# Optimization experiments

Hardware: AMD Instinct MI355X
Metric: run time of the kernel (lower is better)

## Reference

```python
import jax, jax.numpy as jnp
import numpy as np

B, N, K, C_IN, OC = 16, 4096, 16, 64, 64
OC2 = OC // 2
LEAK = 0.2
EPS = 1e-12  # guards sqrt grad when a neighbor equals the center point


def _cbn(x, w, s, b):
    # 1x1 conv (channel-last) + folded eval-mode BatchNorm: (x @ w.T) * s + b
    return jnp.einsum('...i,oi->...o', x, w) * s + b


def _lrelu(x):
    return jax.nn.leaky_relu(x, LEAK)


def _gather(feat, idx):
    # feat [B,N,C], idx [B,N,k] -> [B,N,k,C]  (index_points)
    return jax.vmap(lambda f, i: f[i])(feat, idx)


def _attentive_pool(x_info, feat, idx, wq, sq, bq, wk, sk, bk, wv, sv, bv, w2, s2, b2):
    q = jax.nn.relu(_cbn(feat, wq, sq, bq))   # [B,N,C]
    kf = jax.nn.relu(_cbn(feat, wk, sk, bk))
    vf = jax.nn.relu(_cbn(feat, wv, sv, bv))
    Kn = _gather(kf, idx)                     # [B,N,k,C]
    W = x_info * (Kn - q[:, :, None, :])      # [B,N,k,C]
    Vn = _gather(vf, idx)
    a = jax.nn.softmax(W, axis=2)             # softmax over k neighbors
    out = jnp.sum(a * Vn, axis=2)             # [B,N,C]
    return _lrelu(_cbn(out, w2, s2, b2))


def _forward(x, feature, neighbor_index,
             mlp1_w, mlp1_s, mlp1_b, lse1_w, lse1_s, lse1_b,
             p1_wq, p1_sq, p1_bq, p1_wk, p1_sk, p1_bk, p1_wv, p1_sv, p1_bv, p1_w2, p1_s2, p1_b2,
             lse2_w, lse2_s, lse2_b,
             p2_wq, p2_sq, p2_bq, p2_wk, p2_sk, p2_bk, p2_wv, p2_sv, p2_bv, p2_w2, p2_s2, p2_b2,
             mlp2_w, mlp2_s, mlp2_b, res_w, res_s, res_b):
    idx = neighbor_index
    xt = jnp.transpose(x, (0, 2, 1))          # [B,N,3]
    ft = jnp.transpose(feature, (0, 2, 1))    # [B,N,C_IN]
    identity = ft
    f1 = _lrelu(_cbn(ft, mlp1_w, mlp1_s, mlp1_b))        # [B,N,OC2]
    knn_x = _gather(xt, idx)                             # [B,N,k,3]
    center = jnp.broadcast_to(xt[:, :, None, :], knn_x.shape)
    diff = knn_x - center
    dist = jnp.sqrt(jnp.sum(diff * diff, axis=-1, keepdims=True) + EPS)  # [B,N,k,1]
    x_info = jnp.concatenate([center, knn_x, diff, dist], axis=-1)       # [B,N,k,10]
    x_info = _lrelu(_cbn(x_info, lse1_w, lse1_s, lse1_b))                # [B,N,k,OC2]
    feat2 = _attentive_pool(x_info, f1, idx,
                            p1_wq, p1_sq, p1_bq, p1_wk, p1_sk, p1_bk,
                            p1_wv, p1_sv, p1_bv, p1_w2, p1_s2, p1_b2)    # [B,N,OC2]
    x_info2 = _lrelu(_cbn(x_info, lse2_w, lse2_s, lse2_b))               # [B,N,k,OC2]
    feat3 = _attentive_pool(x_info2, feat2, idx,
                            p2_wq, p2_sq, p2_bq, p2_wk, p2_sk, p2_bk,
                            p2_wv, p2_sv, p2_bv, p2_w2, p2_s2, p2_b2)    # [B,N,OC]
    out = _cbn(feat3, mlp2_w, mlp2_s, mlp2_b)            # [B,N,2*OC]
    res = _cbn(identity, res_w, res_s, res_b)            # [B,N,2*OC]
    out = _lrelu(out + res)
    return jnp.transpose(out, (0, 2, 1))                 # [B,2*OC,N]


def setup_inputs() -> dict:
    key = jax.random.key(0)
    it = iter(jax.random.split(key, 80))
    nxt = lambda: next(it)

    def w(*shape):
        return jax.random.normal(nxt(), shape, jnp.float32) * 0.1

    def bn(c):
        s = jax.random.uniform(nxt(), (c,), jnp.float32, 0.5, 1.5)
        b = jax.random.normal(nxt(), (c,), jnp.float32) * 0.1
        return s, b

    inp = {
        'x': jax.random.normal(nxt(), (B, 3, N), jnp.float32),
        'feature': jax.random.normal(nxt(), (B, C_IN, N), jnp.float32),
        'neighbor_index': jax.random.randint(nxt(), (B, N, K), 0, N, jnp.int32),
    }
    inp['mlp1_w'] = w(OC2, C_IN); inp['mlp1_s'], inp['mlp1_b'] = bn(OC2)
    inp['lse1_w'] = w(OC2, 10); inp['lse1_s'], inp['lse1_b'] = bn(OC2)
    for p, co in (('p1', OC2), ('p2', OC)):
        inp[p + '_wq'] = w(OC2, OC2); inp[p + '_sq'], inp[p + '_bq'] = bn(OC2)
        inp[p + '_wk'] = w(OC2, OC2); inp[p + '_sk'], inp[p + '_bk'] = bn(OC2)
        inp[p + '_wv'] = w(OC2, OC2); inp[p + '_sv'], inp[p + '_bv'] = bn(OC2)
        inp[p + '_w2'] = w(co, OC2); inp[p + '_s2'], inp[p + '_b2'] = bn(co)
    inp['lse2_w'] = w(OC2, OC2); inp['lse2_s'], inp['lse2_b'] = bn(OC2)
    inp['mlp2_w'] = w(2 * OC, OC); inp['mlp2_s'], inp['mlp2_b'] = bn(2 * OC)
    inp['res_w'] = w(2 * OC, C_IN); inp['res_s'], inp['res_b'] = bn(2 * OC)
    return inp


def reference(x, feature, neighbor_index,
              mlp1_w, mlp1_s, mlp1_b, lse1_w, lse1_s, lse1_b,
              p1_wq, p1_sq, p1_bq, p1_wk, p1_sk, p1_bk, p1_wv, p1_sv, p1_bv, p1_w2, p1_s2, p1_b2,
              lse2_w, lse2_s, lse2_b,
              p2_wq, p2_sq, p2_bq, p2_wk, p2_sk, p2_bk, p2_wv, p2_sv, p2_bv, p2_w2, p2_s2, p2_b2,
              mlp2_w, mlp2_s, mlp2_b, res_w, res_s, res_b):
    return _forward(x, feature, neighbor_index,
                    mlp1_w, mlp1_s, mlp1_b, lse1_w, lse1_s, lse1_b,
                    p1_wq, p1_sq, p1_bq, p1_wk, p1_sk, p1_bk, p1_wv, p1_sv, p1_bv, p1_w2, p1_s2, p1_b2,
                    lse2_w, lse2_s, lse2_b,
                    p2_wq, p2_sq, p2_bq, p2_wk, p2_sk, p2_bk, p2_wv, p2_sv, p2_bv, p2_w2, p2_s2, p2_b2,
                    mlp2_w, mlp2_s, mlp2_b, res_w, res_s, res_b)
```

## Files before the change

### kernel.cpp

```cpp
#include <hip/hip_runtime.h>
#include <cstdint>
#include <cstddef>

#define NB 16
#define NP 4096
#define KNN 16
#define CIN 64
#define H 32
#define OCC 64
#define PN ((size_t)NB*NP)

__device__ __forceinline__ float lrelu(float v){ return v > 0.f ? v : 0.2f*v; }
__device__ __forceinline__ float reluf(float v){ return v > 0.f ? v : 0.f; }

typedef __attribute__((ext_vector_type(8)))  short bf16x8s;
typedef __attribute__((ext_vector_type(4)))  float f32x4;
typedef __attribute__((ext_vector_type(16))) float f32x16;

__device__ __forceinline__ short f2bf(float f){
    union { float f; unsigned u; } v; v.f = f;
    unsigned r = v.u + 0x7fffu + ((v.u >> 16) & 1u);
    return (short)(r >> 16);
}

__global__ __launch_bounds__(256) void k_pointwise(
    const float* __restrict__ feat, const float* __restrict__ xpos,
    const float* __restrict__ w1, const float* __restrict__ s1, const float* __restrict__ b1,
    const float* __restrict__ wq, const float* __restrict__ sq, const float* __restrict__ bq,
    const float* __restrict__ wk, const float* __restrict__ sk, const float* __restrict__ bk,
    const float* __restrict__ wv, const float* __restrict__ sv, const float* __restrict__ bv,
    float* __restrict__ q1, float* __restrict__ kv1,
    float* __restrict__ xp, short* __restrict__ ftp,
    const float* __restrict__ m2w, const float* __restrict__ m2s, const float* __restrict__ m2b,
    const float* __restrict__ rw, const float* __restrict__ rs, const float* __restrict__ rb,
    const float* __restrict__ p2w2,
    short* __restrict__ wbigW, short* __restrict__ w2bW, float* __restrict__ bbW)
{
    __shared__ unsigned short ftb[64*72];
    __shared__ unsigned short f1b[64*40];
    int t = threadIdx.x;
    int l = t & 63;
    int g = t >> 6;
    int bid = blockIdx.x;
    int b  = bid >> 6;
    int n0 = (bid & 63) * 64;
    int n  = n0 + l;
    size_t p = (size_t)b*NP + n;

    {
        const float* fb = feat + ((size_t)b*CIN)*NP + n;
        float fv[16];
        #pragma unroll
        for (int k=0;k<16;k++) fv[k] = fb[(size_t)(g*16+k)*NP];
        bf16x8s h0, h1;
        #pragma unroll
        for (int i=0;i<8;i++){ h0[i] = f2bf(fv[i]); h1[i] = f2bf(fv[8+i]); }
        *(bf16x8s*)(ftp + p*64 + g*16)     = h0;
        *(bf16x8s*)(ftp + p*64 + g*16 + 8) = h1;
        *(bf16x8s*)&ftb[l*72 + g*16]       = h0;
        *(bf16x8s*)&ftb[l*72 + g*16 + 8]   = h1;
    }
    if (g == 0){
        const float* xb = xpos + (size_t)b*3*NP;
        *(float4*)(xp + 4*p) = make_float4(xb[n], xb[NP+n], xb[2*NP+n], 0.f);
    }
    if (bid == 0){
        int o = t >> 1, half = t & 1;
        const float* srcp = half ? (rw + (size_t)o*64) : (m2w + (size_t)o*64);
        float sc = half ? rs[o] : m2s[o];
        short* dst = wbigW + (size_t)o*128 + half*64;
        #pragma unroll
        for (int j=0;j<64;j+=8){
            bf16x8s v8;
            #pragma unroll
            for (int i=0;i<8;i++) v8[i] = f2bf(srcp[j+i]*sc);
            *(bf16x8s*)(dst + j) = v8;
        }
        if (!half) bbW[o] = m2b[o] + rb[o];
        {
            int i0 = t*8;
            bf16x8s w8;
            #pragma unroll
            for (int i=0;i<8;i++) w8[i] = f2bf(p2w2[i0+i]);
            *(bf16x8s*)(w2bW + i0) = w8;
        }
    }
    __syncthreads();

    int lr = t & 15;
    int kg = (t >> 4) & 3;
    int prow = g*16 + lr;
    size_t pg = (size_t)b*NP + n0 + prow;

    f32x4 Df0 = {0.f,0.f,0.f,0.f}, Df1 = {0.f,0.f,0.f,0.f};
    #pragma unroll
    for (int kk=0; kk<2; kk++){
        bf16x8s Bf = *(const bf16x8s*)&ftb[prow*72 + kk*32 + kg*8];
        {
            int h = lr;
            float sc = s1[h];
            const float* wr = w1 + h*64 + kk*32 + kg*8;
            bf16x8s Aw;
            #pragma unroll
            for (int i=0;i<8;i++) Aw[i] = f2bf(wr[i]*sc);
            Df0 = __builtin_amdgcn_mfma_f32_16x16x32_bf16(Aw, Bf, Df0, 0, 0, 0);
        }
        {
            int h = 16 + lr;
            float sc = s1[h];
            const float* wr = w1 + h*64 + kk*32 + kg*8;
            bf16x8s Aw;
            #pragma unroll
            for (int i=0;i<8;i++) Aw[i] = f2bf(wr[i]*sc);
            Df1 = __builtin_amdgcn_mfma_f32_16x16x32_bf16(Aw, Bf, Df1, 0, 0, 0);
        }
    }
    {
        int ch = kg*4;
        float4 b4 = *(const float4*)(b1 + ch);
        unsigned u0 = (unsigned short)f2bf(lrelu(Df0[0]+b4.x))
                    | ((unsigned)(unsigned short)f2bf(lrelu(Df0[1]+b4.y)) << 16);
        unsigned u1 = (unsigned short)f2bf(lrelu(Df0[2]+b4.z))
                    | ((unsigned)(unsigned short)f2bf(lrelu(Df0[3]+b4.w)) << 16);
        *(uint2*)&f1b[prow*40 + ch] = make_uint2(u0, u1);
    }
    {
        int ch = 16 + kg*4;
        float4 b4 = *(const float4*)(b1 + ch);
        unsigned u0 = (unsigned short)f2bf(lrelu(Df1[0]+b4.x))
                    | ((unsigned)(unsigned short)f2bf(lrelu(Df1[1]+b4.y)) << 16);
        unsigned u1 = (unsigned short)f2bf(lrelu(Df1[2]+b4.z))
                    | ((unsigned)(unsigned short)f2bf(lrelu(Df1[3]+b4.w)) << 16);
        *(uint2*)&f1b[prow*40 + ch] = make_uint2(u0, u1);
    }

    bf16x8s Bq = *(const bf16x8s*)&f1b[prow*40 + kg*8];
    float qv[6][4];
    {
        const float* wsrc[3] = {wq, wk, wv};
        const float* ssrc[3] = {sq, sk, sv};
        const float* bsrc[3] = {bq, bk, bv};
        #pragma unroll
        for (int m3=0; m3<3; m3++){
            #pragma unroll
            for (int mt=0; mt<2; mt++){
                int h = mt*16 + lr;
                float sc = ssrc[m3][h];
                const float* wr = wsrc[m3] + h*32 + kg*8;
                bf16x8s Aw;
                #pragma unroll
                for (int i=0;i<8;i++) Aw[i] = f2bf(wr[i]*sc);
                f32x4 Dq = {0.f,0.f,0.f,0.f};
                Dq = __builtin_amdgcn_mfma_f32_16x16x32_bf16(Aw, Bq, Dq, 0, 0, 0);
                int ch = mt*16 + kg*4;
                float4 b4 = *(const float4*)(bsrc[m3] + ch);
                qv[m3*2+mt][0] = reluf(Dq[0] + b4.x);
                qv[m3*2+mt][1] = reluf(Dq[1] + b4.y);
                qv[m3*2+mt][2] = reluf(Dq[2] + b4.z);
                qv[m3*2+mt][3] = reluf(Dq[3] + b4.w);
            }
        }
    }
    size_t qb = pg*H;
    *(float4*)(q1 + qb + kg*4)      = make_float4(qv[0][0],qv[0][1],qv[0][2],qv[0][3]);
    *(float4*)(q1 + qb + 16 + kg*4) = make_float4(qv[1][0],qv[1][1],qv[1][2],qv[1][3]);
    #pragma unroll
    for (int mt=0; mt<2; mt++){
        int ch = mt*16 + kg*4;
        *(float4*)(kv1 + 2*(qb+ch))     = make_float4(qv[2+mt][0], qv[4+mt][0],
                                                      qv[2+mt][1], qv[4+mt][1]);
        *(float4*)(kv1 + 2*(qb+ch) + 4) = make_float4(qv[2+mt][2], qv[4+mt][2],
                                                      qv[2+mt][3], qv[4+mt][3]);
    }
}

__global__ __launch_bounds__(256) void k_pool1(
    const float* __restrict__ xp, const int* __restrict__ nidx,
    const float* __restrict__ q1, const float* __restrict__ kv1,
    const float* __restrict__ l1w, const float* __restrict__ l1s, const float* __restrict__ l1b,
    const float* __restrict__ w2, const float* __restrict__ s2, const float* __restrict__ b2,
    const float* __restrict__ wq, const float* __restrict__ sq, const float* __restrict__ bq,
    const float* __restrict__ wk, const float* __restrict__ sk, const float* __restrict__ bk,
    const float* __restrict__ wv, const float* __restrict__ sv, const float* __restrict__ bv,
    float* __restrict__ q2, float* __restrict__ kv2)
{
    __shared__ float wl[4][32*36];
    __shared__ float bcp[4][2][32];
    __shared__ float bcf[4][2][32];
    int t = threadIdx.x;
    {
        const float* wsrc[4] = {w2, wq, wk, wv};
        #pragma unroll
        for (int m=0;m<4;m++)
            for (int i=t;i<1024;i+=256)
                wl[m][(i>>5)*36 + (i&31)] = wsrc[m][i];
    }
    __syncthreads();

    int wv_ = t >> 6;
    int l   = t & 63;
    int n_  = l & 31;
    int hi  = l >> 5;
    int bid = blockIdx.x;
    int sb  = ((bid & 7) << 10) | (bid >> 3);
    size_t p0 = (size_t)sb*8 + (size_t)wv_*2;
    int b = (int)(p0 >> 12);

    bf16x8s Bf;
    if (hi == 0){
        #pragma unroll
        for (int i=0;i<8;i++) Bf[i] = f2bf(l1w[n_*10 + i]);
    } else {
        Bf[0] = f2bf(l1w[n_*10 + 8]);
        Bf[1] = f2bf(l1w[n_*10 + 9]);
        #pragma unroll
        for (int i=2;i<8;i++) Bf[i] = 0;
    }

    int ptA  = (l >> 4) & 1;
    int nbrA = l & 15;
    size_t pA = p0 + ptA;
    int idA = nidx[pA*KNN + nbrA];
    float4 cp = *(const float4*)(xp + 4*pA);
    float4 nv = *(const float4*)(xp + 4*((size_t)(b<<12)+idA));
    float dx = nv.x-cp.x, dy = nv.y-cp.y, dz = nv.z-cp.z;
    float dist = sqrtf(dx*dx+dy*dy+dz*dz + 1e-12f);
    bf16x8s A;
    if (hi == 0){
        A[0]=f2bf(cp.x); A[1]=f2bf(cp.y); A[2]=f2bf(cp.z); A[3]=f2bf(nv.x);
        A[4]=f2bf(nv.y); A[5]=f2bf(nv.z); A[6]=f2bf(dx);   A[7]=f2bf(dy);
    } else {
        A[0]=f2bf(dz); A[1]=f2bf(dist);
        A[2]=0; A[3]=0; A[4]=0; A[5]=0; A[6]=0; A[7]=0;
    }

    f32x16 cz = {0.f,0.f,0.f,0.f,0.f,0.f,0.f,0.f,0.f,0.f,0.f,0.f,0.f,0.f,0.f,0.f};
    f32x16 D = __builtin_amdgcn_mfma_f32_32x32x16_bf16(A, Bf, cz, 0, 0, 0);

    float sl1 = l1s[n_], bl1 = l1b[n_];
    const int* irow0 = nidx + p0*KNN;
    float outv[2];
    #pragma unroll
    for (int pt=0; pt<2; pt++){
        size_t p = p0 + pt;
        float qc = q1[p*H + n_];
        int4 idlo = *(const int4*)(irow0 + pt*KNN + 4*hi);
        int4 idhi = *(const int4*)(irow0 + pt*KNN + 8 + 4*hi);
        int ids[8] = {idlo.x,idlo.y,idlo.z,idlo.w, idhi.x,idhi.y,idhi.z,idhi.w};
        float W[8], V[8];
        #pragma unroll
        for (int rr=0; rr<8; rr++){
            float xi = lrelu(D[pt*8+rr]*sl1 + bl1);
            float2 kv = *(const float2*)(kv1 + 2*(((size_t)b*NP + ids[rr])*H + n_));
            W[rr] = xi*(kv.x - qc);
            V[rr] = kv.y;
        }
        float mx = W[0];
        #pragma unroll
        for (int rr=1;rr<8;rr++) mx = fmaxf(mx, W[rr]);
        mx = fmaxf(mx, __shfl_xor(mx, 32, 64));
        float den = 0.f, ac = 0.f;
        #pragma unroll
        for (int rr=0;rr<8;rr++){
            float e = __expf(W[rr]-mx);
            den += e; ac = fmaf(e, V[rr], ac);
        }
        den += __shfl_xor(den, 32, 64);
        ac  += __shfl_xor(ac,  32, 64);
        outv[pt] = ac/den;
    }
    if (l < 32){ bcp[wv_][0][n_] = outv[0]; bcp[wv_][1][n_] = outv[1]; }

    int c = n_;
    float f2a = 0.f;
    #pragma unroll
    for (int jj=0;jj<8;jj++){
        float4 xv = *(const float4*)&bcp[wv_][hi][jj*4];
        float4 w4 = *(const float4*)&wl[0][c*36 + jj*4];
        f2a += w4.x*xv.x + w4.y*xv.y + w4.z*xv.z + w4.w*xv.w;
    }
    float f2 = lrelu(f2a*s2[c] + b2[c]);
    bcf[wv_][hi][c] = f2;

    float aq=0.f, ak=0.f, av=0.f;
    #pragma unroll
    for (int jj=0;jj<8;jj++){
        float4 xv  = *(const float4*)&bcf[wv_][hi][jj*4];
        float4 wq4 = *(const float4*)&wl[1][c*36 + jj*4];
        float4 wk4 = *(const float4*)&wl[2][c*36 + jj*4];
        float4 wv4 = *(const float4*)&wl[3][c*36 + jj*4];
        aq += wq4.x*xv.x + wq4.y*xv.y + wq4.z*xv.z + wq4.w*xv.w;
        ak += wk4.x*xv.x + wk4.y*xv.y + wk4.z*xv.z + wk4.w*xv.w;
        av += wv4.x*xv.x + wv4.y*xv.y + wv4.z*xv.z + wv4.w*xv.w;
    }
    size_t base = (p0 + hi)*H + c;
    q2[base] = reluf(aq*sq[c]+bq[c]);
    *(float2*)(kv2 + 2*base) = make_float2(reluf(ak*sk[c]+bk[c]), reluf(av*sv[c]+bv[c]));
}

__global__ __launch_bounds__(512) void k_pool2(
    const float* __restrict__ xp, const int* __restrict__ nidx,
    const float* __restrict__ q2, const float* __restrict__ kv2,
    const float* __restrict__ l1w, const float* __restrict__ l1s, const float* __restrict__ l1b,
    const float* __restrict__ l2w, const float* __restrict__ l2s, const float* __restrict__ l2b,
    const short* __restrict__ w2bf, const float* __restrict__ s2, const float* __restrict__ b2,
    const short* __restrict__ ftp, const short* __restrict__ wbig, const float* __restrict__ bb,
    float* __restrict__ out)
{
    __shared__ unsigned short xiT[8][32*40];
    __shared__ unsigned short bcb[16][40];
    __shared__ unsigned short xf[16][72];
    int t = threadIdx.x;
    int wv_ = t >> 6;
    int l   = t & 63;
    int n_  = l & 31;
    int hi  = l >> 5;
    int bid = blockIdx.x;
    int sb  = ((bid & 7) << 9) | (bid >> 3);
    size_t pbase = (size_t)sb * 16;
    size_t p0 = pbase + (size_t)wv_*2;
    int b = (int)(pbase >> 12);

    bf16x8s Bf1;
    if (hi == 0){
        #pragma unroll
        for (int i=0;i<8;i++) Bf1[i] = f2bf(l1w[n_*10 + i]);
    } else {
        Bf1[0] = f2bf(l1w[n_*10 + 8]);
        Bf1[1] = f2bf(l1w[n_*10 + 9]);
        #pragma unroll
        for (int i=2;i<8;i++) Bf1[i] = 0;
    }
    int ptA  = (l >> 4) & 1;
    int nbrA = l & 15;
    size_t pA = p0 + ptA;
    int idA = nidx[pA*KNN + nbrA];
    float4 cp = *(const float4*)(xp + 4*pA);
    float4 nv = *(const float4*)(xp + 4*((size_t)(b<<12)+idA));
    float dx = nv.x-cp.x, dy = nv.y-cp.y, dz = nv.z-cp.z;
    float dist = sqrtf(dx*dx+dy*dy+dz*dz + 1e-12f);
    bf16x8s Ag;
    if (hi == 0){
        Ag[0]=f2bf(cp.x); Ag[1]=f2bf(cp.y); Ag[2]=f2bf(cp.z); Ag[3]=f2bf(nv.x);
        Ag[4]=f2bf(nv.y); Ag[5]=f2bf(nv.z); Ag[6]=f2bf(dx);   Ag[7]=f2bf(dy);
    } else {
        Ag[0]=f2bf(dz); Ag[1]=f2bf(dist);
        Ag[2]=0; Ag[3]=0; Ag[4]=0; Ag[5]=0; Ag[6]=0; Ag[7]=0;
    }
    f32x16 cz = {0.f,0.f,0.f,0.f,0.f,0.f,0.f,0.f,0.f,0.f,0.f,0.f,0.f,0.f,0.f,0.f};
    f32x16 D1 = __builtin_amdgcn_mfma_f32_32x32x16_bf16(Ag, Bf1, cz, 0, 0, 0);

    float sl1 = l1s[n_], bl1 = l1b[n_];
    #pragma unroll
    for (int r=0;r<16;r++){
        int m = (r&3) + 8*(r>>2) + 4*hi;
        xiT[wv_][m*40 + n_] = (unsigned short)f2bf(lrelu(D1[r]*sl1 + bl1));
    }
    bf16x8s A20 = *(const bf16x8s*)&xiT[wv_][n_*40 + hi*8];
    bf16x8s A21 = *(const bf16x8s*)&xiT[wv_][n_*40 + 16 + hi*8];
    bf16x8s B0, B1;
    {
        const float* r0 = l2w + n_*32 + hi*8;
        #pragma unroll
        for (int i=0;i<8;i++){ B0[i] = f2bf(r0[i]); B1[i] = f2bf(r0[16+i]); }
    }
    f32x16 D = __builtin_amdgcn_mfma_f32_32x32x16_bf16(A20, B0, cz, 0, 0, 0);
    D = __builtin_amdgcn_mfma_f32_32x32x16_bf16(A21, B1, D, 0, 0, 0);

    float sl2 = l2s[n_], bl2 = l2b[n_];
    const int* irow0 = nidx + p0*KNN;
    float outv[2];
    #pragma unroll
    for (int pt=0; pt<2; pt++){
        size_t p = p0 + pt;
        float qc = q2[p*H + n_];
        int4 idlo = *(const int4*)(irow0 + pt*KNN + 4*hi);
        int4 idhi = *(const int4*)(irow0 + pt*KNN + 8 + 4*hi);
        int ids[8] = {idlo.x,idlo.y,idlo.z,idlo.w, idhi.x,idhi.y,idhi.z,idhi.w};
        float W[8], V[8];
        #pragma unroll
        for (int rr=0; rr<8; rr++){
            float xi2 = lrelu(D[pt*8+rr]*sl2 + bl2);
            float2 kv = *(const float2*)(kv2 + 2*(((size_t)b*NP + ids[rr])*H + n_));
            W[rr] = xi2*(kv.x - qc);
            V[rr] = kv.y;
        }
        float mx = W[0];
        #pragma unroll
        for (int rr=1;rr<8;rr++) mx = fmaxf(mx, W[rr]);
        mx = fmaxf(mx, __shfl_xor(mx, 32, 64));
        float den = 0.f, ac = 0.f;
        #pragma unroll
        for (int rr=0;rr<8;rr++){
            float e = __expf(W[rr]-mx);
            den += e; ac = fmaf(e, V[rr], ac);
        }
        den += __shfl_xor(den, 32, 64);
        ac  += __shfl_xor(ac,  32, 64);
        outv[pt] = ac/den;
    }
    if (l < 32){
        bcb[wv_*2 + 0][n_] = (unsigned short)f2bf(outv[0]);
        bcb[wv_*2 + 1][n_] = (unsigned short)f2bf(outv[1]);
    }
    __syncthreads();

    int lr = l & 15, kg = l >> 4;
    if (wv_ < 4){
        bf16x8s Aw = *(const bf16x8s*)(w2bf + (wv_*16 + lr)*32 + kg*8);
        bf16x8s Bp = *(const bf16x8s*)&bcb[lr][kg*8];
        f32x4 zz = {0.f,0.f,0.f,0.f};
        f32x4 Df = __builtin_amdgcn_mfma_f32_16x16x32_bf16(Aw, Bp, zz, 0, 0, 0);
        int ch0 = wv_*16 + kg*4;
        float4 s4 = *(const float4*)(s2 + ch0);
        float4 b4 = *(const float4*)(b2 + ch0);
        xf[lr][ch0+0] = (unsigned short)f2bf(lrelu(Df[0]*s4.x + b4.x));
        xf[lr][ch0+1] = (unsigned short)f2bf(lrelu(Df[1]*s4.y + b4.y));
        xf[lr][ch0+2] = (unsigned short)f2bf(lrelu(Df[2]*s4.z + b4.z));
        xf[lr][ch0+3] = (unsigned short)f2bf(lrelu(Df[3]*s4.w + b4.w));
    }
    __syncthreads();

    int o0 = wv_ * 16;
    const short* wr = wbig + (size_t)(o0 + lr)*128 + kg*8;
    bf16x8s Af0 = *(const bf16x8s*)(wr);
    bf16x8s Af1 = *(const bf16x8s*)(wr + 32);
    bf16x8s Af2 = *(const bf16x8s*)(wr + 64);
    bf16x8s Af3 = *(const bf16x8s*)(wr + 96);
    bf16x8s Bx0 = *(const bf16x8s*)&xf[lr][kg*8];
    bf16x8s Bx1 = *(const bf16x8s*)&xf[lr][32 + kg*8];
    const short* fr = ftp + (pbase + lr)*64 + kg*8;
    bf16x8s Bx2 = *(const bf16x8s*)(fr);
    bf16x8s Bx3 = *(const bf16x8s*)(fr + 32);
    f32x4 Dq = {0.f,0.f,0.f,0.f};
    Dq = __builtin_amdgcn_mfma_f32_16x16x32_bf16(Af0, Bx0, Dq, 0, 0, 0);
    Dq = __builtin_amdgcn_mfma_f32_16x16x32_bf16(Af1, Bx1, Dq, 0, 0, 0);
    Dq = __builtin_amdgcn_mfma_f32_16x16x32_bf16(Af2, Bx2, Dq, 0, 0, 0);
    Dq = __builtin_amdgcn_mfma_f32_16x16x32_bf16(Af3, Bx3, Dq, 0, 0, 0);
    float4 bb4 = *(const float4*)(bb + o0 + kg*4);
    int n0 = (int)(pbase & (NP-1));
    float* ob = out + ((size_t)b*128)*NP + n0 + lr;
    ob[(size_t)(o0 + kg*4 + 0)*NP] = lrelu(Dq[0] + bb4.x);
    ob[(size_t)(o0 + kg*4 + 1)*NP] = lrelu(Dq[1] + bb4.y);
    ob[(size_t)(o0 + kg*4 + 2)*NP] = lrelu(Dq[2] + bb4.z);
    ob[(size_t)(o0 + kg*4 + 3)*NP] = lrelu(Dq[3] + bb4.w);
}

extern "C" void kernel_launch(void* const* d_in, const int* in_sizes, int n_in,
                              void* d_out, int out_size, void* d_ws, size_t ws_size,
                              hipStream_t stream)
{
    (void)in_sizes; (void)n_in; (void)out_size; (void)ws_size;
    const float* x     = (const float*)d_in[0];
    const float* feat  = (const float*)d_in[1];
    const int*   nidx  = (const int*)  d_in[2];
    const float* m1w=(const float*)d_in[3],  *m1s=(const float*)d_in[4],  *m1b=(const float*)d_in[5];
    const float* l1w=(const float*)d_in[6],  *l1s=(const float*)d_in[7],  *l1b=(const float*)d_in[8];
    const float* p1wq=(const float*)d_in[9],  *p1sq=(const float*)d_in[10], *p1bq=(const float*)d_in[11];
    const float* p1wk=(const float*)d_in[12], *p1sk=(const float*)d_in[13], *p1bk=(const float*)d_in[14];
    const float* p1wv=(const float*)d_in[15], *p1sv=(const float*)d_in[16], *p1bv=(const float*)d_in[17];
    const float* p1w2=(const float*)d_in[18], *p1s2=(const float*)d_in[19], *p1b2=(const float*)d_in[20];
    const float* p2wq=(const float*)d_in[21], *p2sq=(const float*)d_in[22], *p2bq=(const float*)d_in[23];
    const float* p2wk=(const float*)d_in[24], *p2sk=(const float*)d_in[25], *p2bk=(const float*)d_in[26];
    const float* p2wv=(const float*)d_in[27], *p2sv=(const float*)d_in[28], *p2bv=(const float*)d_in[29];
    const float* p2w2=(const float*)d_in[30], *p2s2=(const float*)d_in[31], *p2b2=(const float*)d_in[32];
    const float* l2w=(const float*)d_in[33], *l2s=(const float*)d_in[34], *l2b=(const float*)d_in[35];
    const float* m2w=(const float*)d_in[36], *m2s=(const float*)d_in[37], *m2b=(const float*)d_in[38];
    const float* rw =(const float*)d_in[39], *rs =(const float*)d_in[40], *rb =(const float*)d_in[41];

    float* ws = (float*)d_ws;
    float* q1  = ws;
    float* kv1 = ws + PN*32;
    float* q2  = ws + PN*96;
    float* kv2 = ws + PN*128;
    float* xp  = ws + PN*192;
    short* ftp = (short*)(ws + PN*196);
    short* wbig = (short*)(ws + PN*228);
    short* w2bf = wbig + 16384;
    float* bb   = (float*)(w2bf + 2048);

    float* outp = (float*)d_out;

    k_pointwise<<<dim3(PN/64),dim3(256),0,stream>>>(feat, x, m1w,m1s,m1b,
        p1wq,p1sq,p1bq, p1wk,p1sk,p1bk, p1wv,p1sv,p1bv, q1,kv1, xp, ftp,
        m2w,m2s,m2b, rw,rs,rb, p2w2, wbig, w2bf, bb);
    k_pool1<<<dim3(PN/8),dim3(256),0,stream>>>(xp,nidx, q1,kv1,
        l1w,l1s,l1b, p1w2,p1s2,p1b2,
        p2wq,p2sq,p2bq, p2wk,p2sk,p2bk, p2wv,p2sv,p2bv, q2,kv2);
    k_pool2<<<dim3(PN/16),dim3(512),0,stream>>>(xp,nidx, q2,kv2,
        l1w,l1s,l1b, l2w,l2s,l2b, w2bf, p2s2, p2b2, ftp, wbig, bb, outp);
}
```

Measured before the change: 294.6 us.

## Move pool1 post-projections to bf16 MFMA and pre-convert weights once

The pool1 kernel now uses 512-thread blocks covering 16 points. Its w2 projection and the following q/k/v projections run as 16x16x32 bf16 MFMAs over shared-memory tiles, replacing per-lane fp32 dot products read from weights staged in LDS. Weight conversion to bf16, with the BN scales folded in, moves into the pointwise kernel and is written once to workspace, so pool1 and pool2 no longer reconvert l1w and l2w per wave. This trades some precision in the f2 and q/k/v projections for less ALU work, and adds block-wide syncs plus scattered strided kv2 stores.

```diff
diff --git a/kernel.cpp b/kernel.cpp
--- a/kernel.cpp
+++ b/kernel.cpp
@@ -34,7 +34,14 @@
     const float* __restrict__ m2w, const float* __restrict__ m2s, const float* __restrict__ m2b,
     const float* __restrict__ rw, const float* __restrict__ rs, const float* __restrict__ rb,
     const float* __restrict__ p2w2,
-    short* __restrict__ wbigW, short* __restrict__ w2bW, float* __restrict__ bbW)
+    const float* __restrict__ l1w, const float* __restrict__ l2w,
+    const float* __restrict__ p1w2, const float* __restrict__ p1s2,
+    const float* __restrict__ w2q, const float* __restrict__ s2q,
+    const float* __restrict__ w2k, const float* __restrict__ s2k,
+    const float* __restrict__ w2v, const float* __restrict__ s2v,
+    short* __restrict__ wbigW, short* __restrict__ w2bW, float* __restrict__ bbW,
+    short* __restrict__ l1wbW, short* __restrict__ l2wbW,
+    short* __restrict__ p1w2bW, short* __restrict__ pqkvbW)
 {
     __shared__ unsigned short ftb[64*72];
     __shared__ unsigned short f1b[64*40];
@@ -83,6 +90,30 @@
             #pragma unroll
             for (int i=0;i<8;i++) w8[i] = f2bf(p2w2[i0+i]);
             *(bf16x8s*)(w2bW + i0) = w8;
+        }
+        if (t < 32){
+            #pragma unroll
+            for (int j=0;j<16;j++)
+                l1wbW[t*16+j] = (j<10) ? f2bf(l1w[t*10+j]) : (short)0;
+        }
+        if (t < 128){
+            int c = t >> 2;
+            int i0 = t*8;
+            bf16x8s a8, c8, q8, k8, v8;
+            float scw = p1s2[c], scq = s2q[c], sck = s2k[c], scv = s2v[c];
+            #pragma unroll
+            for (int i=0;i<8;i++){
+                a8[i] = f2bf(l2w[i0+i]);
+                c8[i] = f2bf(p1w2[i0+i]*scw);
+                q8[i] = f2bf(w2q[i0+i]*scq);
+                k8[i] = f2bf(w2k[i0+i]*sck);
+                v8[i] = f2bf(w2v[i0+i]*scv);
+            }
+            *(bf16x8s*)(l2wbW  + i0) = a8;
+            *(bf16x8s*)(p1w2bW + i0) = c8;
+            *(bf16x8s*)(pqkvbW + i0)        = q8;
+            *(bf16x8s*)(pqkvbW + 1024 + i0) = k8;
+            *(bf16x8s*)(pqkvbW + 2048 + i0) = v8;
         }
     }
     __syncthreads();
@@ -174,48 +205,30 @@
     }
 }
 
-__global__ __launch_bounds__(256) void k_pool1(
+__global__ __launch_bounds__(512) void k_pool1(
     const float* __restrict__ xp, const int* __restrict__ nidx,
     const float* __restrict__ q1, const float* __restrict__ kv1,
-    const float* __restrict__ l1w, const float* __restrict__ l1s, const float* __restrict__ l1b,
-    const float* __restrict__ w2, const float* __restrict__ s2, const float* __restrict__ b2,
-    const float* __restrict__ wq, const float* __restrict__ sq, const float* __restrict__ bq,
-    const float* __restrict__ wk, const float* __restrict__ sk, const float* __restrict__ bk,
-    const float* __restrict__ wv, const float* __restrict__ sv, const float* __restrict__ bv,
+    const short* __restrict__ l1wb,
+    const float* __restrict__ l1s, const float* __restrict__ l1b,
+    const short* __restrict__ p1w2b, const float* __restrict__ b2,
+    const short* __restrict__ pqkvb,
+    const float* __restrict__ bq, const float* __restrict__ bk, const float* __restrict__ bv,
     float* __restrict__ q2, float* __restrict__ kv2)
 {
-    __shared__ float wl[4][32*36];
-    __shared__ float bcp[4][2][32];
-    __shared__ float bcf[4][2][32];
+    __shared__ unsigned short bcb[16][40];
+    __shared__ unsigned short f2t[16][40];
     int t = threadIdx.x;
-    {
-        const float* wsrc[4] = {w2, wq, wk, wv};
-        #pragma unroll
-        for (int m=0;m<4;m++)
-            for (int i=t;i<1024;i+=256)
-                wl[m][(i>>5)*36 + (i&31)] = wsrc[m][i];
-    }
-    __syncthreads();
-
     int wv_ = t >> 6;
     int l   = t & 63;
     int n_  = l & 31;
     int hi  = l >> 5;
     int bid = blockIdx.x;
-    int sb  = ((bid & 7) << 10) | (bid >> 3);
-    size_t p0 = (size_t)sb*8 + (size_t)wv_*2;
-    int b = (int)(p0 >> 12);
-
-    bf16x8s Bf;
-    if (hi == 0){
-        #pragma unroll
-        for (int i=0;i<8;i++) Bf[i] = f2bf(l1w[n_*10 + i]);
-    } else {
-        Bf[0] = f2bf(l1w[n_*10 + 8]);
-        Bf[1] = f2bf(l1w[n_*10 + 9]);
-        #pragma unroll
-        for (int i=2;i<8;i++) Bf[i] = 0;
-    }
+    int sb  = ((bid & 7) << 9) | (bid >> 3);
+    size_t pbase = (size_t)sb * 16;
+    size_t p0 = pbase + (size_t)wv_*2;
+    int b = (int)(pbase >> 12);
+
+    bf16x8s Bf = *(const bf16x8s*)(l1wb + n_*16 + hi*8);
 
     int ptA  = (l >> 4) & 1;
     int nbrA = l & 15;
@@ -269,40 +282,62 @@
         ac  += __shfl_xor(ac,  32, 64);
         outv[pt] = ac/den;
     }
-    if (l < 32){ bcp[wv_][0][n_] = outv[0]; bcp[wv_][1][n_] = outv[1]; }
-
-    int c = n_;
-    float f2a = 0.f;
-    #pragma unroll
-    for (int jj=0;jj<8;jj++){
-        float4 xv = *(const float4*)&bcp[wv_][hi][jj*4];
-        float4 w4 = *(const float4*)&wl[0][c*36 + jj*4];
-        f2a += w4.x*xv.x + w4.y*xv.y + w4.z*xv.z + w4.w*xv.w;
-    }
-    float f2 = lrelu(f2a*s2[c] + b2[c]);
-    bcf[wv_][hi][c] = f2;
-
-    float aq=0.f, ak=0.f, av=0.f;
-    #pragma unroll
-    for (int jj=0;jj<8;jj++){
-        float4 xv  = *(const float4*)&bcf[wv_][hi][jj*4];
-        float4 wq4 = *(const float4*)&wl[1][c*36 + jj*4];
-        float4 wk4 = *(const float4*)&wl[2][c*36 + jj*4];
-        float4 wv4 = *(const float4*)&wl[3][c*36 + jj*4];
-        aq += wq4.x*xv.x + wq4.y*xv.y + wq4.z*xv.z + wq4.w*xv.w;
-        ak += wk4.x*xv.x + wk4.y*xv.y + wk4.z*xv.z + wk4.w*xv.w;
-        av += wv4.x*xv.x + wv4.y*xv.y + wv4.z*xv.z + wv4.w*xv.w;
-    }
-    size_t base = (p0 + hi)*H + c;
-    q2[base] = reluf(aq*sq[c]+bq[c]);
-    *(float2*)(kv2 + 2*base) = make_float2(reluf(ak*sk[c]+bk[c]), reluf(av*sv[c]+bv[c]));
+    if (l < 32){
+        bcb[wv_*2 + 0][n_] = (unsigned short)f2bf(outv[0]);
+        bcb[wv_*2 + 1][n_] = (unsigned short)f2bf(outv[1]);
+    }
+    __syncthreads();
+
+    int lr = l & 15, kg = l >> 4;
+    if (wv_ < 2){
+        bf16x8s Aw = *(const bf16x8s*)(p1w2b + (wv_*16 + lr)*32 + kg*8);
+        bf16x8s Bp = *(const bf16x8s*)&bcb[lr][kg*8];
+        f32x4 Df = {0.f,0.f,0.f,0.f};
+        Df = __builtin_amdgcn_mfma_f32_16x16x32_bf16(Aw, Bp, Df, 0, 0, 0);
+        int ch0 = wv_*16 + kg*4;
+        float4 b4 = *(const float4*)(b2 + ch0);
+        f2t[lr][ch0+0] = (unsigned short)f2bf(lrelu(Df[0] + b4.x));
+        f2t[lr][ch0+1] = (unsigned short)f2bf(lrelu(Df[1] + b4.y));
+        f2t[lr][ch0+2] = (unsigned short)f2bf(lrelu(Df[2] + b4.z));
+        f2t[lr][ch0+3] = (unsigned short)f2bf(lrelu(Df[3] + b4.w));
+    }
+    __syncthreads();
+
+    if (wv_ < 6){
+        int m3 = wv_ >> 1, mt = wv_ & 1;
+        bf16x8s Aw = *(const bf16x8s*)(pqkvb + m3*1024 + (mt*16 + lr)*32 + kg*8);
+        bf16x8s Bp = *(const bf16x8s*)&f2t[lr][kg*8];
+        f32x4 Dq = {0.f,0.f,0.f,0.f};
+        Dq = __builtin_amdgcn_mfma_f32_16x16x32_bf16(Aw, Bp, Dq, 0, 0, 0);
+        int ch0 = mt*16 + kg*4;
+        size_t p = pbase + lr;
+        if (m3 == 0){
+            float4 b4 = *(const float4*)(bq + ch0);
+            *(float4*)(q2 + p*H + ch0) = make_float4(
+                reluf(Dq[0]+b4.x), reluf(Dq[1]+b4.y), reluf(Dq[2]+b4.z), reluf(Dq[3]+b4.w));
+        } else if (m3 == 1){
+            float4 b4 = *(const float4*)(bk + ch0);
+            kv2[2*(p*H + ch0 + 0)] = reluf(Dq[0]+b4.x);
+            kv2[2*(p*H + ch0 + 1)] = reluf(Dq[1]+b4.y);
+            kv2[2*(p*H + ch0 + 2)] = reluf(Dq[2]+b4.z);
+            kv2[2*(p*H + ch0 + 3)] = reluf(Dq[3]+b4.w);
+        } else {
+            float4 b4 = *(const float4*)(bv + ch0);
+            kv2[2*(p*H + ch0 + 0) + 1] = reluf(Dq[0]+b4.x);
+            kv2[2*(p*H + ch0 + 1) + 1] = reluf(Dq[1]+b4.y);
+            kv2[2*(p*H + ch0 + 2) + 1] = reluf(Dq[2]+b4.z);
+            kv2[2*(p*H + ch0 + 3) + 1] = reluf(Dq[3]+b4.w);
+        }
+    }
 }
 
 __global__ __launch_bounds__(512) void k_pool2(
     const float* __restrict__ xp, const int* __restrict__ nidx,
     const float* __restrict__ q2, const float* __restrict__ kv2,
-    const float* __restrict__ l1w, const float* __restrict__ l1s, const float* __restrict__ l1b,
-    const float* __restrict__ l2w, const float* __restrict__ l2s, const float* __restrict__ l2b,
+    const short* __restrict__ l1wb,
+    const float* __restrict__ l1s, const float* __restrict__ l1b,
+    const short* __restrict__ l2wb,
+    const float* __restrict__ l2s, const float* __restrict__ l2b,
     const short* __restrict__ w2bf, const float* __restrict__ s2, const float* __restrict__ b2,
     const short* __restrict__ ftp, const short* __restrict__ wbig, const float* __restrict__ bb,
     float* __restrict__ out)
@@ -321,16 +356,7 @@
     size_t p0 = pbase + (size_t)wv_*2;
     int b = (int)(pbase >> 12);
 
-    bf16x8s Bf1;
-    if (hi == 0){
-        #pragma unroll
-        for (int i=0;i<8;i++) Bf1[i] = f2bf(l1w[n_*10 + i]);
-    } else {
-        Bf1[0] = f2bf(l1w[n_*10 + 8]);
-        Bf1[1] = f2bf(l1w[n_*10 + 9]);
-        #pragma unroll
-        for (int i=2;i<8;i++) Bf1[i] = 0;
-    }
+    bf16x8s Bf1 = *(const bf16x8s*)(l1wb + n_*16 + hi*8);
     int ptA  = (l >> 4) & 1;
     int nbrA = l & 15;
     size_t pA = p0 + ptA;
@@ -358,12 +384,8 @@
     }
     bf16x8s A20 = *(const bf16x8s*)&xiT[wv_][n_*40 + hi*8];
     bf16x8s A21 = *(const bf16x8s*)&xiT[wv_][n_*40 + 16 + hi*8];
-    bf16x8s B0, B1;
-    {
-        const float* r0 = l2w + n_*32 + hi*8;
-        #pragma unroll
-        for (int i=0;i<8;i++){ B0[i] = f2bf(r0[i]); B1[i] = f2bf(r0[16+i]); }
-    }
+    bf16x8s B0 = *(const bf16x8s*)(l2wb + n_*32 + hi*8);
+    bf16x8s B1 = *(const bf16x8s*)(l2wb + n_*32 + 16 + hi*8);
     f32x16 D = __builtin_amdgcn_mfma_f32_32x32x16_bf16(A20, B0, cz, 0, 0, 0);
     D = __builtin_amdgcn_mfma_f32_32x32x16_bf16(A21, B1, D, 0, 0, 0);
 
@@ -475,18 +497,23 @@
     float* kv2 = ws + PN*128;
     float* xp  = ws + PN*192;
     short* ftp = (short*)(ws + PN*196);
-    short* wbig = (short*)(ws + PN*228);
-    short* w2bf = wbig + 16384;
-    float* bb   = (float*)(w2bf + 2048);
+    short* wbig  = (short*)(ws + PN*228);
+    short* w2bf  = wbig + 16384;
+    float* bb    = (float*)(w2bf + 2048);
+    short* l1wb  = (short*)(bb + 128);
+    short* l2wb  = l1wb + 512;
+    short* p1w2b = l2wb + 1024;
+    short* pqkvb = p1w2b + 1024;
 
     float* outp = (float*)d_out;
 
     k_pointwise<<<dim3(PN/64),dim3(256),0,stream>>>(feat, x, m1w,m1s,m1b,
         p1wq,p1sq,p1bq, p1wk,p1sk,p1bk, p1wv,p1sv,p1bv, q1,kv1, xp, ftp,
-        m2w,m2s,m2b, rw,rs,rb, p2w2, wbig, w2bf, bb);
-    k_pool1<<<dim3(PN/8),dim3(256),0,stream>>>(xp,nidx, q1,kv1,
-        l1w,l1s,l1b, p1w2,p1s2,p1b2,
-        p2wq,p2sq,p2bq, p2wk,p2sk,p2bk, p2wv,p2sv,p2bv, q2,kv2);
+        m2w,m2s,m2b, rw,rs,rb, p2w2,
+        l1w, l2w, p1w2, p1s2, p2wq,p2sq, p2wk,p2sk, p2wv,p2sv,
+        wbig, w2bf, bb, l1wb, l2wb, p1w2b, pqkvb);
+    k_pool1<<<dim3(PN/16),dim3(512),0,stream>>>(xp,nidx, q1,kv1,
+        l1wb, l1s,l1b, p1w2b, p1b2, pqkvb, p2bq,p2bk,p2bv, q2,kv2);
     k_pool2<<<dim3(PN/16),dim3(512),0,stream>>>(xp,nidx, q2,kv2,
-        l1w,l1s,l1b, l2w,l2s,l2b, w2bf, p2s2, p2b2, ftp, wbig, bb, outp);
+        l1wb, l1s,l1b, l2wb, l2s,l2b, w2bf, p2s2, p2b2, ftp, wbig, bb, outp);
 }
```

Result: faster. 261.9 us (-11.1%).
